# Performance work log

Hardware: AMD Instinct MI355X
Metric: run time of the kernel (lower is better)

## Reference

```python
import jax, jax.numpy as jnp
import numpy as np

DIM = 384
H = W = 56
WS = 7
SS = 3
NH = 12
NMLP = 1536
N = WS * WS  # 49 tokens per window
EPS = 1e-5


def _rel_pos_index(ws):
    coords = np.stack(np.meshgrid(np.arange(ws), np.arange(ws), indexing='ij')).reshape(2, -1)
    rel = (coords[:, :, None] - coords[:, None, :]).transpose(1, 2, 0)
    rel[:, :, 0] += ws - 1
    rel[:, :, 1] += ws - 1
    rel[:, :, 0] *= 2 * ws - 1
    return rel.sum(-1)  # (N, N) int


def _attn_mask(Hh, Ww, ws, ss):
    img = np.zeros((Hh, Ww), dtype=np.float32)
    cnt = 0
    for h in (slice(0, -ws), slice(-ws, -ss), slice(-ss, None)):
        for w in (slice(0, -ws), slice(-ws, -ss), slice(-ss, None)):
            img[h, w] = cnt
            cnt += 1
    mw = img.reshape(Hh // ws, ws, Ww // ws, ws).transpose(0, 2, 1, 3).reshape(-1, ws * ws)
    diff = mw[:, None, :] - mw[:, :, None]  # (nW, N, N)
    return np.where(diff != 0, np.float32(-100.0), np.float32(0.0))


_REL_IDX = jnp.asarray(_rel_pos_index(WS))          # (49, 49)
_MASK = jnp.asarray(_attn_mask(H, W, WS, SS))       # (64, 49, 49)


def _ln(x, g, b):
    mu = jnp.mean(x, axis=-1, keepdims=True)
    var = jnp.mean(jnp.square(x - mu), axis=-1, keepdims=True)
    return (x - mu) * jax.lax.rsqrt(var + EPS) * g + b


def setup_inputs() -> dict:
    key = jax.random.key(0)
    ks = jax.random.split(key, 8)
    s = 0.02
    return {
        'x': jax.random.normal(ks[0], (32, H * W, DIM), dtype=jnp.float32),
        'g1': jnp.ones((DIM,), jnp.float32),
        'be1': jnp.zeros((DIM,), jnp.float32),
        'w_qkv': jax.random.normal(ks[1], (DIM, 3 * DIM), jnp.float32) * s,
        'b_qkv': jnp.zeros((3 * DIM,), jnp.float32),
        'rel_table': jax.random.normal(ks[2], ((2 * WS - 1) ** 2, NH), jnp.float32) * s,
        'w_proj': jax.random.normal(ks[3], (DIM, DIM), jnp.float32) * s,
        'b_proj': jnp.zeros((DIM,), jnp.float32),
        'g2': jnp.ones((DIM,), jnp.float32),
        'be2': jnp.zeros((DIM,), jnp.float32),
        'w1': jax.random.normal(ks[4], (DIM, NMLP), jnp.float32) * s,
        'b1': jnp.zeros((NMLP,), jnp.float32),
        'w2': jax.random.normal(ks[5], (NMLP, DIM), jnp.float32) * s,
        'b2': jnp.zeros((DIM,), jnp.float32),
    }


def reference(x, g1, be1, w_qkv, b_qkv, rel_table, w_proj, b_proj, g2, be2, w1, b1, w2, b2):
    B, L, C = x.shape
    hd = C // NH
    scale = hd ** -0.5

    shortcut = x
    h = _ln(x, g1, be1).reshape(B, H, W, C)
    h = jnp.roll(h, (-SS, -SS), axis=(1, 2))
    # window partition -> (B*nW, N, C)
    xw = h.reshape(B, H // WS, WS, W // WS, WS, C).transpose(0, 1, 3, 2, 4, 5).reshape(-1, N, C)
    B_ = xw.shape[0]

    qkv = (xw @ w_qkv + b_qkv).reshape(B_, N, 3, NH, hd).transpose(2, 0, 3, 1, 4)
    q, k, v = qkv[0], qkv[1], qkv[2]  # (B_, NH, N, hd)
    attn = jnp.einsum('whid,whjd->whij', q, k) * scale  # (B_, NH, N, N)

    bias = rel_table[_REL_IDX.reshape(-1)].reshape(N, N, NH).transpose(2, 0, 1)
    attn = attn + bias[None]

    nW = _MASK.shape[0]
    attn = attn.reshape(B_ // nW, nW, NH, N, N) + _MASK[None, :, None]
    attn = attn.reshape(B_, NH, N, N)
    attn = jax.nn.softmax(attn, axis=-1)

    out = jnp.einsum('whij,whjd->whid', attn, v).transpose(0, 2, 1, 3).reshape(B_, N, C)
    out = out @ w_proj + b_proj

    # window reverse -> (B, H, W, C)
    out = out.reshape(B, H // WS, W // WS, WS, WS, C).transpose(0, 1, 3, 2, 4, 5).reshape(B, H, W, C)
    out = jnp.roll(out, (SS, SS), axis=(1, 2)).reshape(B, L, C)

    x1 = out + shortcut
    m = _ln(x1, g2, be2)
    m = jax.nn.gelu(m @ w1 + b1, approximate=False) @ w2 + b2
    return m + x1
```

## Files before the change

kernel.cpp:

```cpp
#include <hip/hip_runtime.h>
#include <hip/hip_bf16.h>
#include <math.h>

typedef __attribute__((ext_vector_type(8))) short bf16x8;
typedef __attribute__((ext_vector_type(4))) short bf16x4;
typedef __attribute__((ext_vector_type(4))) float f32x4;
typedef __hip_bfloat16 bf16;

#define NH 12
#define HD 32
#define NPAD 64
#define NWIN 2048
#define NTOK 100352
#define HBLK (NPAD*HD)
#define WBLK (3*NH*HBLK)

typedef __attribute__((address_space(3))) const void cv3;

#define STR2(x) #x
#define DSR(dst, base, OFF)                                                  \
  asm volatile("ds_read_b128 %0, %1 offset:" STR2(OFF)                       \
               : "=v"(dst) : "v"(base))

__device__ inline float wave_sum(float v) {
#pragma unroll
  for (int off = 32; off; off >>= 1) v += __shfl_xor(v, off);
  return v;
}

__device__ inline void load_lds16(const bf16* g, bf16* l) {
  __builtin_amdgcn_global_load_lds((const __attribute__((address_space(1))) void*)g,
                                   (__attribute__((address_space(3))) void*)l, 16, 0, 0);
}

__device__ inline short bfbits(float f) {
  bf16 h = __float2bfloat16(f);
  return *(short*)&h;
}

__global__ __launch_bounds__(256) void cast_transpose(const float* __restrict__ in,
                                                      bf16* __restrict__ out, int K, int N) {
  int e = blockIdx.x * 256 + threadIdx.x;
  if (e >= K * N) return;
  int n = e / K, k = e - n * K;
  out[e] = __float2bfloat16(in[k * N + n]);
}

__global__ __launch_bounds__(256) void zero_pads(bf16* __restrict__ qkv) {
  int idx = blockIdx.x * 256 + threadIdx.x;
  const int total = NWIN * 3 * NH * 15 * HD;
  if (idx >= total) return;
  int d = idx & 31; int rest = idx >> 5;
  int n = 49 + (rest % 15); rest /= 15;
  int h = rest % NH; rest /= NH;
  int which = rest % 3; int w = rest / 3;
  size_t base = (size_t)w * WBLK + (size_t)which * NH * HBLK + (size_t)h * HBLK;
  size_t addr = (which == 2) ? base + (size_t)d * NPAD + n : base + (size_t)n * HD + d;
  qkv[addr] = __float2bfloat16(0.0f);
}

__global__ __launch_bounds__(256) void build_bias(const float* __restrict__ rel,
                                                  float* __restrict__ tbl) {
  int e = blockIdx.x * 256 + threadIdx.x;
  if (e >= 4 * 12 * 49 * 64) return;
  int col = e & 63; int t = e >> 6;
  int row = t % 49; t /= 49;
  int h = t % 12; int cls = t / 12;
  float v;
  if (col >= 49) {
    v = -1e30f;
  } else {
    int py = row / 7, px = row - py * 7;
    int qy = col / 7, qx = col - qy * 7;
    int ridx = (py - qy + 6) * 13 + (px - qx + 6);
    v = rel[ridx * 12 + h];
    int wy7 = cls >> 1, wx7 = cls & 1;
    int ly_r = wy7 ? (py < 4 ? 1 : 2) : 0;
    int lx_r = wx7 ? (px < 4 ? 1 : 2) : 0;
    int ly_c = wy7 ? (qy < 4 ? 1 : 2) : 0;
    int lx_c = wx7 ? (qx < 4 ? 1 : 2) : 0;
    if ((ly_r * 3 + lx_r) != (ly_c * 3 + lx_c)) v += -100.0f;
  }
  tbl[e] = v;
}

template <int MODE>
__global__ __launch_bounds__(256) void ln_kernel(const float* __restrict__ x,
                                                 const float* __restrict__ g,
                                                 const float* __restrict__ be,
                                                 bf16* __restrict__ out) {
  int wv = threadIdx.x >> 6, lane = threadIdx.x & 63;
  int t = blockIdx.x * 4 + wv;
  size_t src;
  if (MODE == 0) {
    int w = t / 49, n = t - w * 49;
    int b = w >> 6, wi = w & 63;
    int wy = wi >> 3, wx = wi & 7;
    int py = n / 7, px = n - py * 7;
    int rr = wy * 7 + py, cc = wx * 7 + px;
    int ro = rr + 3; if (ro >= 56) ro -= 56;
    int co = cc + 3; if (co >= 56) co -= 56;
    src = (size_t)b * 3136 + ro * 56 + co;
  } else {
    src = (size_t)t;
  }
  const float2* row2 = (const float2*)(x + src * 384);
  float2 v[3]; float s = 0.f;
#pragma unroll
  for (int j = 0; j < 3; ++j) { v[j] = row2[lane + 64 * j]; s += v[j].x + v[j].y; }
  s = wave_sum(s);
  float mu = s * (1.f / 384.f);
  float q = 0.f;
#pragma unroll
  for (int j = 0; j < 3; ++j) {
    float dx = v[j].x - mu, dy = v[j].y - mu;
    q += dx * dx + dy * dy;
  }
  q = wave_sum(q);
  float rs = rsqrtf(q * (1.f / 384.f) + 1e-5f);
  uint* o = (uint*)(out + (size_t)t * 384);
  const float2* g2 = (const float2*)g;
  const float2* b2 = (const float2*)be;
#pragma unroll
  for (int j = 0; j < 3; ++j) {
    int c2 = lane + 64 * j;
    float2 gg = g2[c2], bb = b2[c2];
    float ox = (v[j].x - mu) * rs * gg.x + bb.x;
    float oy = (v[j].y - mu) * rs * gg.y + bb.y;
    o[c2] = (uint)(unsigned short)bfbits(ox) | ((uint)(unsigned short)bfbits(oy) << 16);
  }
}

template <int EPI>
__global__ __launch_bounds__(256, 4) void gemm128(const bf16* __restrict__ A,
                                                  const bf16* __restrict__ BT,
                                                  int K, int NCOL, int row0,
                                                  const float* __restrict__ bias,
                                                  const float* __restrict__ extra,
                                                  void* __restrict__ outp) {
  __shared__ __align__(16) bf16 As[2][128 * 32];
  __shared__ __align__(16) bf16 Bs[2][128 * 32];
  int tid = threadIdx.x, lane = tid & 63, wv = tid >> 6;
  int wr = wv >> 1, wc = wv & 1;
  int lr = lane & 15, lg = lane >> 4;

  int nwg = gridDim.x;
  int bid = blockIdx.x;
  int xcd = bid & 7, li = bid >> 3;
  int qq = nwg >> 3, rr8 = nwg & 7;
  int start = xcd * qq + (xcd < rr8 ? xcd : rr8);
  int lin = start + li;
  int brow = lin / NCOL, bcol = lin - brow * NCOL;

  const bf16* Ab = A + (size_t)brow * 128 * K;
  const bf16* Bb = BT + (size_t)bcol * 128 * K;

  int srow = lane >> 2;
  int scol8 = (((lane & 3) ^ ((srow >> 1) & 3)) << 3);
  const bf16* aS = Ab + (size_t)(wv * 32 + srow) * K + scol8;
  const bf16* bS = Bb + (size_t)(wv * 32 + srow) * K + scol8;

  f32x4 acc[4][4] = {};
  int nk = K >> 5;
  int koff = ((lg ^ ((lr >> 1) & 3)) << 3);

#define STAGE(buf)                                                            \
  {                                                                           \
    load_lds16(aS, &As[buf][wv * 1024]);                                      \
    load_lds16(aS + (size_t)16 * K, &As[buf][wv * 1024 + 512]);               \
    load_lds16(bS, &Bs[buf][wv * 1024]);                                      \
    load_lds16(bS + (size_t)16 * K, &Bs[buf][wv * 1024 + 512]);               \
    aS += 32; bS += 32;                                                       \
  }

  STAGE(0);
  asm volatile("s_waitcnt vmcnt(0)" ::: "memory");
  __builtin_amdgcn_s_barrier();

  for (int it = 0; it < nk; ++it) {
    int buf = it & 1;
    if (it + 1 < nk) STAGE(buf ^ 1);
    cv3* pA = (cv3*)&As[buf][(wr * 64 + lr) * 32 + koff];
    cv3* pB = (cv3*)&Bs[buf][(wc * 64 + lr) * 32 + koff];
    bf16x8 a[4], b[4];
    DSR(a[0], pA, 0);
    DSR(b[0], pB, 0); DSR(b[1], pB, 1024); DSR(b[2], pB, 2048); DSR(b[3], pB, 3072);
    DSR(a[1], pA, 1024); DSR(a[2], pA, 2048); DSR(a[3], pA, 3072);
    asm volatile("s_waitcnt lgkmcnt(3)" ::: "memory");
    __builtin_amdgcn_sched_barrier(0);
    __builtin_amdgcn_s_setprio(1);
#pragma unroll
    for (int j = 0; j < 4; ++j)
      acc[0][j] = __builtin_amdgcn_mfma_f32_16x16x32_bf16(b[j], a[0], acc[0][j], 0, 0, 0);
    __builtin_amdgcn_s_setprio(0);
    asm volatile("s_waitcnt lgkmcnt(0)" ::: "memory");
    __builtin_amdgcn_sched_barrier(0);
    __builtin_amdgcn_s_setprio(1);
#pragma unroll
    for (int i = 1; i < 4; ++i)
#pragma unroll
      for (int j = 0; j < 4; ++j)
        acc[i][j] = __builtin_amdgcn_mfma_f32_16x16x32_bf16(b[j], a[i], acc[i][j], 0, 0, 0);
    __builtin_amdgcn_s_setprio(0);
    if (it + 1 < nk) {
      asm volatile("s_waitcnt vmcnt(0)" ::: "memory");
      __builtin_amdgcn_s_barrier();
    }
  }
#undef STAGE

  float4 bias4[4];
#pragma unroll
  for (int j = 0; j < 4; ++j)
    bias4[j] = *(const float4*)(bias + bcol * 128 + wc * 64 + j * 16 + lg * 4);

#pragma unroll
  for (int i = 0; i < 4; ++i) {
    int lrow = brow * 128 + wr * 64 + i * 16 + lr;
    int grow = row0 + lrow;
    int w_ = 0, n_ = 0; size_t tok = 0;
    if (EPI == 0 || EPI == 1) {
      w_ = grow / 49; n_ = grow - w_ * 49;
      if (EPI == 1) {
        int b_ = w_ >> 6, wi = w_ & 63;
        int wy = wi >> 3, wx = wi & 7;
        int py = n_ / 7, px = n_ - py * 7;
        int r2 = wy * 7 + py, c2 = wx * 7 + px;
        int ro = r2 + 3; if (ro >= 56) ro -= 56;
        int co = c2 + 3; if (co >= 56) co -= 56;
        tok = (size_t)b_ * 3136 + ro * 56 + co;
      }
    }
#pragma unroll
    for (int j = 0; j < 4; ++j) {
      int col = bcol * 128 + wc * 64 + j * 16 + lg * 4;
      float v0 = acc[i][j][0] + bias4[j].x;
      float v1 = acc[i][j][1] + bias4[j].y;
      float v2 = acc[i][j][2] + bias4[j].z;
      float v3 = acc[i][j][3] + bias4[j].w;
      if (EPI == 0) {
        int which = (col >= 768) ? 2 : (col >= 384 ? 1 : 0);
        int cc = col - which * 384;
        int hh = cc >> 5, d0 = cc & 31;
        size_t base = (size_t)w_ * WBLK + (size_t)which * NH * HBLK + (size_t)hh * HBLK;
        if (which == 2) {
          bf16* vp = (bf16*)outp + base + (size_t)d0 * NPAD + n_;
          vp[0] = __float2bfloat16(v0);
          vp[NPAD] = __float2bfloat16(v1);
          vp[2 * NPAD] = __float2bfloat16(v2);
          vp[3 * NPAD] = __float2bfloat16(v3);
        } else {
          bf16x4 p = {bfbits(v0), bfbits(v1), bfbits(v2), bfbits(v3)};
          *(bf16x4*)((bf16*)outp + base + (size_t)n_ * HD + d0) = p;
        }
      } else if (EPI == 1) {
        size_t oidx = tok * 384 + col;
        float4 e = *(const float4*)(extra + oidx);
        float4 o = {v0 + e.x, v1 + e.y, v2 + e.z, v3 + e.w};
        *(float4*)((float*)outp + oidx) = o;
      } else if (EPI == 2) {
        float g0 = 0.5f * v0 * (1.0f + erff(v0 * 0.70710678118654752f));
        float g1 = 0.5f * v1 * (1.0f + erff(v1 * 0.70710678118654752f));
        float g2 = 0.5f * v2 * (1.0f + erff(v2 * 0.70710678118654752f));
        float g3 = 0.5f * v3 * (1.0f + erff(v3 * 0.70710678118654752f));
        bf16x4 p = {bfbits(g0), bfbits(g1), bfbits(g2), bfbits(g3)};
        *(bf16x4*)((bf16*)outp + (size_t)lrow * 1536 + col) = p;
      } else {
        size_t oidx = (size_t)grow * 384 + col;
        float4 e = *(const float4*)(extra + oidx);
        float4 o = {v0 + e.x, v1 + e.y, v2 + e.z, v3 + e.w};
        *(float4*)((float*)outp + oidx) = o;
      }
    }
  }
}

__global__ __launch_bounds__(256) void attn_kernel(const bf16* __restrict__ qkv,
                                                   const float* __restrict__ tbl,
                                                   bf16* __restrict__ attn_out) {
  __shared__ __align__(16) bf16 P[4][64 * 72];
  int wv = threadIdx.x >> 6, lane = threadIdx.x & 63;
  int lr = lane & 15, lg = lane >> 4;
  int w = blockIdx.x;
  int wi = w & 63, wy = wi >> 3, wx = wi & 7;
  int cls = ((wy == 7) ? 2 : 0) | ((wx == 7) ? 1 : 0);
  const bf16* base = qkv + (size_t)w * WBLK;
  bf16* Pl = &P[wv][0];
  const float scale = 0.17677669529663689f;

  for (int hh = 0; hh < 3; ++hh) {
    int h = wv + hh * 4;
    const bf16* Q  = base + (size_t)h * HBLK;
    const bf16* Kp = base + (size_t)(NH + h) * HBLK;
    const bf16* Vt = base + (size_t)(2 * NH + h) * HBLK;
    const float* tb = tbl + (size_t)(cls * 12 + h) * 49 * 64;

    bf16x8 qa[4], kb[4];
#pragma unroll
    for (int t = 0; t < 4; ++t) {
      qa[t] = *(const bf16x8*)(Q  + (t * 16 + lr) * 32 + lg * 8);
      kb[t] = *(const bf16x8*)(Kp + (t * 16 + lr) * 32 + lg * 8);
    }
    f32x4 S[4][4] = {};
#pragma unroll
    for (int i = 0; i < 4; ++i)
#pragma unroll
      for (int j = 0; j < 4; ++j)
        S[i][j] = __builtin_amdgcn_mfma_f32_16x16x32_bf16(qa[i], kb[j], S[i][j], 0, 0, 0);

#pragma unroll
    for (int i = 0; i < 4; ++i) {
#pragma unroll
      for (int r = 0; r < 4; ++r) {
        int row = i * 16 + lg * 4 + r;
        const float* trow = tb + (row < 49 ? row : 0) * 64;
        float sv[4]; float m = -1e30f;
#pragma unroll
        for (int j = 0; j < 4; ++j) {
          float s = S[i][j][r] * scale + trow[j * 16 + lr];
          sv[j] = s;
          m = fmaxf(m, s);
        }
        m = fmaxf(m, __shfl_xor(m, 1));
        m = fmaxf(m, __shfl_xor(m, 2));
        m = fmaxf(m, __shfl_xor(m, 4));
        m = fmaxf(m, __shfl_xor(m, 8));
        float ev[4]; float sum = 0.f;
#pragma unroll
        for (int j = 0; j < 4; ++j) { ev[j] = __expf(sv[j] - m); sum += ev[j]; }
        sum += __shfl_xor(sum, 1);
        sum += __shfl_xor(sum, 2);
        sum += __shfl_xor(sum, 4);
        sum += __shfl_xor(sum, 8);
        float inv = 1.0f / sum;
#pragma unroll
        for (int j = 0; j < 4; ++j)
          Pl[row * 72 + j * 16 + lr] = __float2bfloat16(ev[j] * inv);
      }
    }

    bf16x8 vb[2][2];
#pragma unroll
    for (int kt = 0; kt < 2; ++kt)
#pragma unroll
      for (int cj = 0; cj < 2; ++cj)
        vb[kt][cj] = *(const bf16x8*)(Vt + (cj * 16 + lr) * 64 + kt * 32 + lg * 8);
    f32x4 O[4][2] = {};
#pragma unroll
    for (int i = 0; i < 4; ++i) {
#pragma unroll
      for (int kt = 0; kt < 2; ++kt) {
        bf16x8 pa = *(const bf16x8*)(Pl + (i * 16 + lr) * 72 + kt * 32 + lg * 8);
#pragma unroll
        for (int cj = 0; cj < 2; ++cj)
          O[i][cj] = __builtin_amdgcn_mfma_f32_16x16x32_bf16(pa, vb[kt][cj], O[i][cj], 0, 0, 0);
      }
    }
#pragma unroll
    for (int i = 0; i < 4; ++i)
#pragma unroll
      for (int cj = 0; cj < 2; ++cj)
#pragma unroll
        for (int r = 0; r < 4; ++r) {
          int n = i * 16 + lg * 4 + r;
          if (n < 49)
            attn_out[((size_t)w * 49 + n) * 384 + h * 32 + cj * 16 + lr] =
                __float2bfloat16(O[i][cj][r]);
        }
  }
}

extern "C" void kernel_launch(void* const* d_in, const int* in_sizes, int n_in,
                              void* d_out, int out_size, void* d_ws, size_t ws_size,
                              hipStream_t stream) {
  (void)in_sizes; (void)n_in; (void)out_size;
  const float* x     = (const float*)d_in[0];
  const float* g1    = (const float*)d_in[1];
  const float* be1   = (const float*)d_in[2];
  const float* w_qkv = (const float*)d_in[3];
  const float* b_qkv = (const float*)d_in[4];
  const float* rel   = (const float*)d_in[5];
  const float* w_pr  = (const float*)d_in[6];
  const float* b_pr  = (const float*)d_in[7];
  const float* g2    = (const float*)d_in[8];
  const float* be2   = (const float*)d_in[9];
  const float* w1    = (const float*)d_in[10];
  const float* b1    = (const float*)d_in[11];
  const float* w2    = (const float*)d_in[12];
  const float* b2    = (const float*)d_in[13];
  float* out = (float*)d_out;

  if (ws_size < 390070272u) return;

  char* ws = (char*)d_ws;
  bf16* wqkvT = (bf16*)(ws);
  bf16* wprT  = (bf16*)(ws + 884736);
  bf16* w1T   = (bf16*)(ws + 1179648);
  bf16* w2T   = (bf16*)(ws + 2359296);
  float* btbl = (float*)(ws + 3538944);
  bf16* xw    = (bf16*)(ws + (4u << 20));
  bf16* qkv   = (bf16*)(ws + (84u << 20));
  bf16* m_in  = qkv;
  bf16* h1    = (bf16*)(ws + (164u << 20));

  cast_transpose<<<dim3((442368 + 255) / 256), 256, 0, stream>>>(w_qkv, wqkvT, 384, 1152);
  cast_transpose<<<dim3((147456 + 255) / 256), 256, 0, stream>>>(w_pr, wprT, 384, 384);
  cast_transpose<<<dim3((589824 + 255) / 256), 256, 0, stream>>>(w1, w1T, 384, 1536);
  cast_transpose<<<dim3((589824 + 255) / 256), 256, 0, stream>>>(w2, w2T, 1536, 384);

  build_bias<<<dim3((4 * 12 * 49 * 64 + 255) / 256), 256, 0, stream>>>(rel, btbl);

  zero_pads<<<dim3((NWIN * 3 * NH * 15 * HD + 255) / 256), 256, 0, stream>>>(qkv);

  ln_kernel<0><<<dim3(NTOK / 4), 256, 0, stream>>>(x, g1, be1, xw);

  gemm128<0><<<dim3(7056), 256, 0, stream>>>(xw, wqkvT, 384, 9, 0, b_qkv, nullptr,
                                             (void*)qkv);

  attn_kernel<<<dim3(NWIN), 256, 0, stream>>>(qkv, btbl, xw);

  gemm128<1><<<dim3(2352), 256, 0, stream>>>(xw, wprT, 384, 3, 0, b_pr, x, (void*)out);

  ln_kernel<1><<<dim3(NTOK / 4), 256, 0, stream>>>(out, g2, be2, m_in);

  for (int c = 0; c < 2; ++c) {
    gemm128<2><<<dim3(4704), 256, 0, stream>>>(m_in + (size_t)c * 50176 * 384, w1T, 384,
                                               12, c * 50176, b1, nullptr, (void*)h1);
    gemm128<3><<<dim3(1176), 256, 0, stream>>>(h1, w2T, 1536, 3, c * 50176, b2, out,
                                               (void*)out);
  }
}
```

Before: 956.4 us.

## Add triple-buffered GEMM for MLP down-projection and unchunk the MLP

Adds a dedicated fc2 GEMM kernel with a three-stage LDS pipeline, XCD-aware block remapping and a fused bias plus residual epilogue. It replaces the generic gemm128 EPI 3 path for that matmul. The MLP no longer runs in two token chunks: the full fc1 output is written in one launch and consumed by the new kernel in one launch, and workspace buffers are re-laid out so they fit. The aim is to hide global-load latency on the K=1536 GEMM and to cut launch and tail overhead. The cost is more LDS per block and a larger hidden-activation buffer.

```diff
diff --git a/kernel.cpp b/kernel.cpp
--- a/kernel.cpp
+++ b/kernel.cpp
@@ -258,19 +258,115 @@
         float4 e = *(const float4*)(extra + oidx);
         float4 o = {v0 + e.x, v1 + e.y, v2 + e.z, v3 + e.w};
         *(float4*)((float*)outp + oidx) = o;
-      } else if (EPI == 2) {
+      } else {
         float g0 = 0.5f * v0 * (1.0f + erff(v0 * 0.70710678118654752f));
         float g1 = 0.5f * v1 * (1.0f + erff(v1 * 0.70710678118654752f));
         float g2 = 0.5f * v2 * (1.0f + erff(v2 * 0.70710678118654752f));
         float g3 = 0.5f * v3 * (1.0f + erff(v3 * 0.70710678118654752f));
         bf16x4 p = {bfbits(g0), bfbits(g1), bfbits(g2), bfbits(g3)};
         *(bf16x4*)((bf16*)outp + (size_t)lrow * 1536 + col) = p;
-      } else {
-        size_t oidx = (size_t)grow * 384 + col;
-        float4 e = *(const float4*)(extra + oidx);
-        float4 o = {v0 + e.x, v1 + e.y, v2 + e.z, v3 + e.w};
-        *(float4*)((float*)outp + oidx) = o;
       }
+    }
+  }
+}
+
+__global__ __launch_bounds__(256, 3) void gemm3s(const bf16* __restrict__ A,
+                                                 const bf16* __restrict__ BT,
+                                                 int K, int NCOL, int row0,
+                                                 const float* __restrict__ bias,
+                                                 const float* __restrict__ extra,
+                                                 float* __restrict__ outp) {
+  __shared__ __align__(16) bf16 As[3][128 * 32];
+  __shared__ __align__(16) bf16 Bs[3][128 * 32];
+  int tid = threadIdx.x, lane = tid & 63, wv = tid >> 6;
+  int wr = wv >> 1, wc = wv & 1;
+  int lr = lane & 15, lg = lane >> 4;
+
+  int nwg = gridDim.x;
+  int bid = blockIdx.x;
+  int xcd = bid & 7, li = bid >> 3;
+  int qq = nwg >> 3, rr8 = nwg & 7;
+  int start = xcd * qq + (xcd < rr8 ? xcd : rr8);
+  int lin = start + li;
+  int brow = lin / NCOL, bcol = lin - brow * NCOL;
+
+  const bf16* Ab = A + (size_t)brow * 128 * K;
+  const bf16* Bb = BT + (size_t)bcol * 128 * K;
+
+  int srow = lane >> 2;
+  int scol8 = (((lane & 3) ^ ((srow >> 1) & 3)) << 3);
+  const bf16* aS = Ab + (size_t)(wv * 32 + srow) * K + scol8;
+  const bf16* bS = Bb + (size_t)(wv * 32 + srow) * K + scol8;
+
+  f32x4 acc[4][4] = {};
+  int nk = K >> 5;
+  int koff = ((lg ^ ((lr >> 1) & 3)) << 3);
+
+#define STAGE3(buf)                                                           \
+  {                                                                           \
+    load_lds16(aS, &As[buf][wv * 1024]);                                      \
+    load_lds16(aS + (size_t)16 * K, &As[buf][wv * 1024 + 512]);               \
+    load_lds16(bS, &Bs[buf][wv * 1024]);                                      \
+    load_lds16(bS + (size_t)16 * K, &Bs[buf][wv * 1024 + 512]);               \
+    aS += 32; bS += 32;                                                       \
+  }
+
+  STAGE3(0);
+  STAGE3(1);
+  asm volatile("s_waitcnt vmcnt(4)" ::: "memory");
+  __builtin_amdgcn_s_barrier();
+
+  for (int it = 0; it < nk; ++it) {
+    int buf = it % 3;
+    if (it + 2 < nk) STAGE3((it + 2) % 3);
+    cv3* pA = (cv3*)&As[buf][(wr * 64 + lr) * 32 + koff];
+    cv3* pB = (cv3*)&Bs[buf][(wc * 64 + lr) * 32 + koff];
+    bf16x8 a[4], b[4];
+    DSR(a[0], pA, 0);
+    DSR(b[0], pB, 0); DSR(b[1], pB, 1024); DSR(b[2], pB, 2048); DSR(b[3], pB, 3072);
+    DSR(a[1], pA, 1024); DSR(a[2], pA, 2048); DSR(a[3], pA, 3072);
+    asm volatile("s_waitcnt lgkmcnt(3)" ::: "memory");
+    __builtin_amdgcn_sched_barrier(0);
+    __builtin_amdgcn_s_setprio(1);
+#pragma unroll
+    for (int j = 0; j < 4; ++j)
+      acc[0][j] = __builtin_amdgcn_mfma_f32_16x16x32_bf16(b[j], a[0], acc[0][j], 0, 0, 0);
+    __builtin_amdgcn_s_setprio(0);
+    asm volatile("s_waitcnt lgkmcnt(0)" ::: "memory");
+    __builtin_amdgcn_sched_barrier(0);
+    __builtin_amdgcn_s_setprio(1);
+#pragma unroll
+    for (int i = 1; i < 4; ++i)
+#pragma unroll
+      for (int j = 0; j < 4; ++j)
+        acc[i][j] = __builtin_amdgcn_mfma_f32_16x16x32_bf16(b[j], a[i], acc[i][j], 0, 0, 0);
+    __builtin_amdgcn_s_setprio(0);
+    if (it + 1 < nk) {
+      if (it + 2 < nk)
+        asm volatile("s_waitcnt vmcnt(4)" ::: "memory");
+      else
+        asm volatile("s_waitcnt vmcnt(0)" ::: "memory");
+      __builtin_amdgcn_s_barrier();
+    }
+  }
+#undef STAGE3
+
+  float4 bias4[4];
+#pragma unroll
+  for (int j = 0; j < 4; ++j)
+    bias4[j] = *(const float4*)(bias + bcol * 128 + wc * 64 + j * 16 + lg * 4);
+
+#pragma unroll
+  for (int i = 0; i < 4; ++i) {
+    int grow = row0 + brow * 128 + wr * 64 + i * 16 + lr;
+#pragma unroll
+    for (int j = 0; j < 4; ++j) {
+      int col = bcol * 128 + wc * 64 + j * 16 + lg * 4;
+      size_t oidx = (size_t)grow * 384 + col;
+      float4 e = *(const float4*)(extra + oidx);
+      float4 o = {acc[i][j][0] + bias4[j].x + e.x, acc[i][j][1] + bias4[j].y + e.y,
+                  acc[i][j][2] + bias4[j].z + e.z, acc[i][j][3] + bias4[j].w + e.w};
+      *(float4*)(outp + oidx) = o;
     }
   }
 }
@@ -390,7 +486,7 @@
   const float* b2    = (const float*)d_in[13];
   float* out = (float*)d_out;
 
-  if (ws_size < 390070272u) return;
+  if (ws_size < 389545984u) return;
 
   char* ws = (char*)d_ws;
   bf16* wqkvT = (bf16*)(ws);
@@ -399,9 +495,9 @@
   bf16* w2T   = (bf16*)(ws + 2359296);
   float* btbl = (float*)(ws + 3538944);
   bf16* xw    = (bf16*)(ws + (4u << 20));
+  bf16* m_in  = xw;
   bf16* qkv   = (bf16*)(ws + (84u << 20));
-  bf16* m_in  = qkv;
-  bf16* h1    = (bf16*)(ws + (164u << 20));
+  bf16* h1    = (bf16*)(ws + 81264640u);
 
   cast_transpose<<<dim3((442368 + 255) / 256), 256, 0, stream>>>(w_qkv, wqkvT, 384, 1152);
   cast_transpose<<<dim3((147456 + 255) / 256), 256, 0, stream>>>(w_pr, wprT, 384, 384);
@@ -423,10 +519,7 @@
 
   ln_kernel<1><<<dim3(NTOK / 4), 256, 0, stream>>>(out, g2, be2, m_in);
 
-  for (int c = 0; c < 2; ++c) {
-    gemm128<2><<<dim3(4704), 256, 0, stream>>>(m_in + (size_t)c * 50176 * 384, w1T, 384,
-                                               12, c * 50176, b1, nullptr, (void*)h1);
-    gemm128<3><<<dim3(1176), 256, 0, stream>>>(h1, w2T, 1536, 3, c * 50176, b2, out,
-                                               (void*)out);
-  }
-}
+  gemm128<2><<<dim3(9408), 256, 0, stream>>>(m_in, w1T, 384, 12, 0, b1, nullptr, (void*)h1);
+
+  gemm3s<<<dim3(2352), 256, 0, stream>>>(h1, w2T, 1536, 3, 0, b2, out, out);
+}
```

After: 939.1 us. About the same (-1.8%).
